# Kernel optimization log

Measured on AMD Instinct MI355X. Metric: run time of the kernel, lower is better.

## Reference

```python
import jax, jax.numpy as jnp
import numpy as np

D = 1024
H = 16
K = 32768
EPS = 1e-5


def setup_inputs() -> dict:
    key = jax.random.key(0)
    ks = jax.random.split(key, 12)
    s = 1.0 / np.sqrt(D)
    return {
        "query": jax.random.normal(ks[0], (D,), jnp.float32),
        "neighbors": jax.random.normal(ks[1], (K, D), jnp.float32),
        # nn.MultiheadAttention params
        "in_proj_w": jax.random.uniform(ks[2], (3 * D, D), jnp.float32, -s, s),
        "in_proj_b": jnp.zeros((3 * D,), jnp.float32),
        "out_proj_w": jax.random.uniform(ks[3], (D, D), jnp.float32, -s, s),
        "out_proj_b": jnp.zeros((D,), jnp.float32),
        # FFN params
        "w1": jax.random.uniform(ks[4], (4 * D, D), jnp.float32, -s, s),
        "b1": jnp.zeros((4 * D,), jnp.float32),
        "w2": jax.random.uniform(ks[5], (D, 4 * D), jnp.float32, -s, s),
        "b2": jnp.zeros((D,), jnp.float32),
        # LayerNorm params
        "g1": jnp.ones((D,), jnp.float32),
        "be1": jnp.zeros((D,), jnp.float32),
        "g2": jnp.ones((D,), jnp.float32),
        "be2": jnp.zeros((D,), jnp.float32),
    }


def _layernorm(x, g, b):
    m = jnp.mean(x, axis=-1, keepdims=True)
    v = jnp.var(x, axis=-1, keepdims=True)
    return (x - m) * jax.lax.rsqrt(v + EPS) * g + b


def reference(query, neighbors, in_proj_w, in_proj_b, out_proj_w, out_proj_b,
              w1, b1, w2, b2, g1, be1, g2, be2):
    dh = D // H
    wq, wk, wv = in_proj_w[:D], in_proj_w[D:2 * D], in_proj_w[2 * D:]
    bq, bk, bv = in_proj_b[:D], in_proj_b[D:2 * D], in_proj_b[2 * D:]

    q = (query @ wq.T + bq).reshape(H, dh)            # [H, dh]
    k = (neighbors @ wk.T + bk).reshape(K, H, dh)     # [K, H, dh]
    v = (neighbors @ wv.T + bv).reshape(K, H, dh)

    scores = jnp.einsum('hd,khd->hk', q, k) / np.sqrt(dh)  # [H, K]
    attn = jax.nn.softmax(scores, axis=-1)
    ctx = jnp.einsum('hk,khd->hd', attn, v).reshape(D)      # [D]
    attn_out = ctx @ out_proj_w.T + out_proj_b

    x = _layernorm(query + attn_out, g1, be1)
    ffn = jax.nn.gelu(x @ w1.T + b1, approximate=False) @ w2.T + b2
    return _layernorm(x + ffn, g2, be2)
```

## Files before the change

### kernel.cpp

```cpp
#include <hip/hip_runtime.h>
#include <hip/hip_bf16.h>

#define D 1024
#define H 16
#define DH 64
#define KN 32768
#define EPS 1e-5f

__device__ __forceinline__ float wave_sum(float v){
  #pragma unroll
  for (int off = 32; off; off >>= 1) v += __shfl_xor(v, off, 64);
  return v;
}

#define GLL(gp, lp) __builtin_amdgcn_global_load_lds((const __attribute__((address_space(1))) void*)(gp), (__attribute__((address_space(3))) void*)(lp), 16, 0, 0)

__global__ void g_qproj(const float* __restrict__ query, const float* __restrict__ ipw,
                        const float* __restrict__ ipb, float* __restrict__ q){
  int j = blockIdx.x, l = threadIdx.x;
  const float4* qv = (const float4*)(query + l*16);
  const float4* wv = (const float4*)(ipw + (size_t)j*D + l*16);
  float acc = 0.f;
  #pragma unroll
  for (int t = 0; t < 4; t++){
    float4 a = qv[t], b = wv[t];
    acc += a.x*b.x + a.y*b.y + a.z*b.z + a.w*b.w;
  }
  acc = wave_sum(acc);
  if (l == 0) q[j] = acc + ipb[j];
}

__global__ __launch_bounds__(256) void g_qk(const float* __restrict__ ipw, const float* __restrict__ ipb,
                                            const float* __restrict__ q, float* __restrict__ qk,
                                            float* __restrict__ sb){
  int b = blockIdx.x, t = threadIdx.x;
  int h = b >> 2, sl = b & 3;
  int jg = t >> 6, c = t & 63;
  __shared__ float qh[DH];
  __shared__ float4 red[256];
  if (t < DH) qh[t] = q[h*DH + t];
  __syncthreads();
  if (t < DH){
    float p = qh[t] * ipb[D + h*DH + t];
    p = wave_sum(p);
    if (t == 0 && sl == 0) sb[h] = p;
  }
  float4 acc = make_float4(0.f,0.f,0.f,0.f);
  for (int jj = 0; jj < 16; jj++){
    int j = jg*16 + jj;
    float4 w = *((const float4*)(ipw + (size_t)(D + h*DH + j)*D) + sl*64 + c);
    float qj = qh[j];
    acc.x += qj*w.x; acc.y += qj*w.y; acc.z += qj*w.z; acc.w += qj*w.w;
  }
  red[t] = acc;
  __syncthreads();
  if (jg == 0){
    float4 a = red[c], b1 = red[64+c], c1 = red[128+c], d1 = red[192+c];
    float4 r = make_float4(a.x+b1.x+c1.x+d1.x, a.y+b1.y+c1.y+d1.y,
                           a.z+b1.z+c1.z+d1.z, a.w+b1.w+c1.w+d1.w);
    ((float4*)(qk + h*D))[sl*64 + c] = r;
  }
}

__global__ __launch_bounds__(256, 2) void g_attn(const float* __restrict__ nbr, const float* __restrict__ qk,
                       const float* __restrict__ sb, float* __restrict__ lpart,
                       float* __restrict__ part, int rows_per_blk){
  __shared__ __align__(16) float tile[2][8*D];
  const int t = threadIdx.x;
  const int w = t >> 6, ci = t & 63;
  const int wb = t & ~63;
  const int g = (ci >> 4) & 3;
  const float sbl = sb[w*4 + g];

  float qk0[16], qk1[16], qk2[16], qk3[16];
  {
    const float4* p0 = (const float4*)(qk + (w*4+0)*D);
    const float4* p1 = (const float4*)(qk + (w*4+1)*D);
    const float4* p2 = (const float4*)(qk + (w*4+2)*D);
    const float4* p3 = (const float4*)(qk + (w*4+3)*D);
    #pragma unroll
    for (int c = 0; c < 4; c++){
      float4 f;
      f = p0[c*64 + ci]; qk0[4*c]=f.x; qk0[4*c+1]=f.y; qk0[4*c+2]=f.z; qk0[4*c+3]=f.w;
      f = p1[c*64 + ci]; qk1[4*c]=f.x; qk1[4*c+1]=f.y; qk1[4*c+2]=f.z; qk1[4*c+3]=f.w;
      f = p2[c*64 + ci]; qk2[4*c]=f.x; qk2[4*c+1]=f.y; qk2[4*c+2]=f.z; qk2[4*c+3]=f.w;
      f = p3[c*64 + ci]; qk3[4*c]=f.x; qk3[4*c+1]=f.y; qk3[4*c+2]=f.z; qk3[4*c+3]=f.w;
    }
  }
  float acc0[16], acc1[16], acc2[16], acc3[16];
  #pragma unroll
  for (int i = 0; i < 16; i++){ acc0[i]=0.f; acc1[i]=0.f; acc2[i]=0.f; acc3[i]=0.f; }
  float lsum = 0.f;

  const int k0 = blockIdx.x * rows_per_blk;
  const int ntiles = rows_per_blk >> 3;
  const uint4* gb = (const uint4*)nbr;

  {
    const uint4* gsrc = gb + (size_t)k0*256;
    #pragma unroll
    for (int i = 0; i < 8; i++) GLL(gsrc + i*256 + t, &tile[0][(i*256 + wb)*4]);
  }
  __syncthreads();

  #pragma unroll 1
  for (int tl = 0; tl < ntiles; tl++){
    int cur = tl & 1;
    if (tl + 1 < ntiles){
      const uint4* gsrc = gb + (size_t)(k0 + (tl+1)*8)*256;
      #pragma unroll
      for (int i = 0; i < 8; i++) GLL(gsrc + i*256 + t, &tile[cur^1][(i*256 + wb)*4]);
    }
    #pragma unroll 1
    for (int r = 0; r < 8; r++){
      const float4* row4 = (const float4*)(tile[cur]) + r*256;
      float xf[16];
      float s0=0.f, s1=0.f, s2=0.f, s3=0.f;
      #pragma unroll
      for (int c = 0; c < 4; c++){
        float4 a = row4[c*64 + ci];
        xf[4*c]=a.x; xf[4*c+1]=a.y; xf[4*c+2]=a.z; xf[4*c+3]=a.w;
        s0 += a.x*qk0[4*c] + a.y*qk0[4*c+1] + a.z*qk0[4*c+2] + a.w*qk0[4*c+3];
        s1 += a.x*qk1[4*c] + a.y*qk1[4*c+1] + a.z*qk1[4*c+2] + a.w*qk1[4*c+3];
        s2 += a.x*qk2[4*c] + a.y*qk2[4*c+1] + a.z*qk2[4*c+2] + a.w*qk2[4*c+3];
        s3 += a.x*qk3[4*c] + a.y*qk3[4*c+1] + a.z*qk3[4*c+2] + a.w*qk3[4*c+3];
      }
      const bool lo32 = (ci & 32) == 0;
      float za = lo32 ? s2 : s0;
      float ka = lo32 ? s0 : s2;
      float u02 = ka + __shfl_xor(za, 32, 64);
      float zb = lo32 ? s3 : s1;
      float kb = lo32 ? s1 : s3;
      float u13 = kb + __shfl_xor(zb, 32, 64);
      const bool lo16 = (ci & 16) == 0;
      float zc = lo16 ? u13 : u02;
      float kc = lo16 ? u02 : u13;
      float v = kc + __shfl_xor(zc, 16, 64);
      v += __shfl_xor(v, 8, 64);
      v += __shfl_xor(v, 4, 64);
      v += __shfl_xor(v, 2, 64);
      v += __shfl_xor(v, 1, 64);
      float pv = __expf((v + sbl)*0.125f);
      lsum += pv;
      float p0 = __shfl(pv, 0, 64);
      float p1 = __shfl(pv, 16, 64);
      float p2 = __shfl(pv, 32, 64);
      float p3 = __shfl(pv, 48, 64);
      #pragma unroll
      for (int j = 0; j < 16; j++){
        acc0[j] += p0*xf[j];
        acc1[j] += p1*xf[j];
        acc2[j] += p2*xf[j];
        acc3[j] += p3*xf[j];
      }
    }
    __syncthreads();
  }

  if ((ci & 15) == 0) lpart[blockIdx.x*H + w*4 + g] = lsum;
  float4* o = (float4*)(part + (size_t)blockIdx.x*(H*D) + (size_t)(w*4)*D);
  #pragma unroll
  for (int c = 0; c < 4; c++){
    o[0*256 + c*64 + ci] = make_float4(acc0[4*c], acc0[4*c+1], acc0[4*c+2], acc0[4*c+3]);
    o[1*256 + c*64 + ci] = make_float4(acc1[4*c], acc1[4*c+1], acc1[4*c+2], acc1[4*c+3]);
    o[2*256 + c*64 + ci] = make_float4(acc2[4*c], acc2[4*c+1], acc2[4*c+2], acc2[4*c+3]);
    o[3*256 + c*64 + ci] = make_float4(acc3[4*c], acc3[4*c+1], acc3[4*c+2], acc3[4*c+3]);
  }
}

__global__ __launch_bounds__(256) void g_red(const float* __restrict__ part, const float* __restrict__ lpart,
                                             float* __restrict__ nb, float* __restrict__ lh, int nblk){
  int b = blockIdx.x, t = threadIdx.x;
  __shared__ float red[256];
  if (b == 256){
    int h = t & 15, cs = t >> 4;
    int per = nblk >> 4;
    float s = 0.f;
    for (int k = 0; k < per; k++) s += lpart[(cs*per + k)*H + h];
    red[t] = s;
    __syncthreads();
    if (t < 16){
      float a = 0.f;
      #pragma unroll
      for (int i = 0; i < 16; i++) a += red[i*16 + t];
      lh[t] = a;
    }
    return;
  }
  int o0 = b * 64;
  int oo = t & 63, cs = t >> 6;
  int per = nblk >> 2;
  float s = 0.f;
  #pragma unroll 8
  for (int k = 0; k < per; k++) s += part[(size_t)(cs*per + k)*(H*D) + o0 + oo];
  red[t] = s;
  __syncthreads();
  if (t < 64) nb[o0 + t] = red[t] + red[64+t] + red[128+t] + red[192+t];
}

__global__ void g_ctx(const float* __restrict__ ipw, const float* __restrict__ ipb,
                      const float* __restrict__ nb, const float* __restrict__ lh,
                      float* __restrict__ ctx){
  int j = blockIdx.x, l = threadIdx.x, h = j >> 6;
  const float4* wv = (const float4*)(ipw + (size_t)(2*D + j)*D + l*16);
  const float4* nv = (const float4*)(nb + h*D + l*16);
  float acc = 0.f;
  #pragma unroll
  for (int t = 0; t < 4; t++){
    float4 b = wv[t], n = nv[t];
    acc += b.x*n.x + b.y*n.y + b.z*n.z + b.w*n.w;
  }
  acc = wave_sum(acc);
  if (l == 0) ctx[j] = acc/lh[h] + ipb[2*D + j];
}

__global__ void g_attnout(const float* __restrict__ opw, const float* __restrict__ opb,
                          const float* __restrict__ query, const float* __restrict__ ctx,
                          float* __restrict__ xb){
  int j = blockIdx.x, l = threadIdx.x;
  const float4* wv = (const float4*)(opw + (size_t)j*D + l*16);
  const float4* cv = (const float4*)(ctx + l*16);
  float acc = 0.f;
  #pragma unroll
  for (int t = 0; t < 4; t++){
    float4 b = wv[t], c = cv[t];
    acc += b.x*c.x + b.y*c.y + b.z*c.z + b.w*c.w;
  }
  acc = wave_sum(acc);
  if (l == 0) xb[j] = query[j] + acc + opb[j];
}

__global__ __launch_bounds__(256) void g_ffn1(const float* __restrict__ w1, const float* __restrict__ b1,
                                              const float* __restrict__ xb,
                                              const float* __restrict__ g1, const float* __restrict__ be1,
                                              float* __restrict__ xln, float* __restrict__ h1){
  int t = threadIdx.x, b = blockIdx.x;
  __shared__ float xs[D];
  __shared__ float red[8];
  float4 v = ((const float4*)xb)[t];
  float s = wave_sum(v.x + v.y + v.z + v.w);
  if ((t & 63) == 0) red[t >> 6] = s;
  __syncthreads();
  float m = (red[0]+red[1]+red[2]+red[3]) * (1.0f/D);
  float4 d = make_float4(v.x-m, v.y-m, v.z-m, v.w-m);
  float s2 = wave_sum(d.x*d.x + d.y*d.y + d.z*d.z + d.w*d.w);
  if ((t & 63) == 0) red[4 + (t >> 6)] = s2;
  __syncthreads();
  float var = (red[4]+red[5]+red[6]+red[7]) * (1.0f/D);
  float rs = rsqrtf(var + EPS);
  float4 gg = ((const float4*)g1)[t], bb = ((const float4*)be1)[t];
  float4 r = make_float4(d.x*rs*gg.x + bb.x, d.y*rs*gg.y + bb.y,
                         d.z*rs*gg.z + bb.z, d.w*rs*gg.w + bb.w);
  ((float4*)xs)[t] = r;
  if (b == 0) ((float4*)xln)[t] = r;
  __syncthreads();

  int w = t >> 6, l = t & 63;
  const float4* xs4 = (const float4*)xs;
  #pragma unroll 1
  for (int rr = 0; rr < 4; rr++){
    int j = b*16 + w*4 + rr;
    const float4* wr = (const float4*)(w1 + (size_t)j*D);
    float a = 0.f;
    #pragma unroll
    for (int c = 0; c < 4; c++){
      float4 ww = wr[c*64 + l], xx = xs4[c*64 + l];
      a += ww.x*xx.x + ww.y*xx.y + ww.z*xx.z + ww.w*xx.w;
    }
    a = wave_sum(a);
    if (l == 0){
      float z = a + b1[j];
      h1[j] = 0.5f*z*(1.0f + erff(z*0.70710678118654752f));
    }
  }
}

__global__ void g_ffn2(const float* __restrict__ w2, const float* __restrict__ b2v,
                       const float* __restrict__ h1, float* __restrict__ y){
  int j = blockIdx.x, l = threadIdx.x;
  const float4* wv = (const float4*)(w2 + (size_t)j*4096 + l*64);
  const float4* hv = (const float4*)(h1 + l*64);
  float acc = 0.f;
  #pragma unroll
  for (int t = 0; t < 16; t++){
    float4 b = wv[t], hh = hv[t];
    acc += b.x*hh.x + b.y*hh.y + b.z*hh.z + b.w*hh.w;
  }
  acc = wave_sum(acc);
  if (l == 0) y[j] = acc + b2v[j];
}

__global__ __launch_bounds__(1024) void g_ln2(const float* __restrict__ xln, const float* __restrict__ y,
                                              const float* __restrict__ g, const float* __restrict__ be,
                                              float* __restrict__ out){
  int t = threadIdx.x;
  __shared__ float red[16];
  __shared__ float bc;
  float v = xln[t] + y[t];
  float s = wave_sum(v);
  if ((t & 63) == 0) red[t >> 6] = s;
  __syncthreads();
  if (t == 0){ float a = 0.f; for (int i = 0; i < 16; i++) a += red[i]; bc = a*(1.0f/D); }
  __syncthreads();
  float m = bc;
  float d = v - m;
  float s2 = wave_sum(d*d);
  if ((t & 63) == 0) red[t >> 6] = s2;
  __syncthreads();
  if (t == 0){ float a = 0.f; for (int i = 0; i < 16; i++) a += red[i]; bc = a*(1.0f/D); }
  __syncthreads();
  float rs = rsqrtf(bc + EPS);
  out[t] = d*rs*g[t] + be[t];
}

extern "C" void kernel_launch(void* const* d_in, const int* in_sizes, int n_in,
                              void* d_out, int out_size, void* d_ws, size_t ws_size,
                              hipStream_t stream) {
  const float* query = (const float*)d_in[0];
  const float* nbr   = (const float*)d_in[1];
  const float* ipw   = (const float*)d_in[2];
  const float* ipb   = (const float*)d_in[3];
  const float* opw   = (const float*)d_in[4];
  const float* opb   = (const float*)d_in[5];
  const float* w1    = (const float*)d_in[6];
  const float* b1    = (const float*)d_in[7];
  const float* w2    = (const float*)d_in[8];
  const float* b2v   = (const float*)d_in[9];
  const float* g1    = (const float*)d_in[10];
  const float* be1   = (const float*)d_in[11];
  const float* g2    = (const float*)d_in[12];
  const float* be2   = (const float*)d_in[13];

  float* ws    = (float*)d_ws;
  float* q     = ws;
  float* qk    = q + D;
  float* sb    = qk + H*D;
  float* lh    = sb + 16;
  float* ctx   = lh + 16;
  float* xb    = ctx + D;
  float* xln   = xb + D;
  float* h1    = xln + D;
  float* y     = h1 + 4*D;
  float* nb    = y + D;
  float* lpart = nb + H*D;
  float* part  = lpart + 8192;

  size_t fixed_bytes = (size_t)(part - ws) * 4;
  int nblk = 512;
  while (nblk > 64 && fixed_bytes + (size_t)nblk*H*D*4 > ws_size) nblk >>= 1;
  int rows_per_blk = KN / nblk;

  g_qproj  <<<1024, 64, 0, stream>>>(query, ipw, ipb, q);
  g_qk     <<<64, 256, 0, stream>>>(ipw, ipb, q, qk, sb);
  g_attn   <<<nblk, 256, 0, stream>>>(nbr, qk, sb, lpart, part, rows_per_blk);
  g_red    <<<257, 256, 0, stream>>>(part, lpart, nb, lh, nblk);
  g_ctx    <<<1024, 64, 0, stream>>>(ipw, ipb, nb, lh, ctx);
  g_attnout<<<1024, 64, 0, stream>>>(opw, opb, query, ctx, xb);
  g_ffn1   <<<256, 256, 0, stream>>>(w1, b1, xb, g1, be1, xln, h1);
  g_ffn2   <<<1024, 64, 0, stream>>>(w2, b2v, h1, y);
  g_ln2    <<<1, 1024, 0, stream>>>(xln, y, g2, be2, (float*)d_out);
}
```

Before: 299.4 us.

## Fuse q projection into qk kernel, pair rows in attention loop, widen reduction

Merges the query projection kernel into the qk kernel, with each block recomputing its head's 64 q values, which removes one launch. The attention inner loop now handles two rows per iteration so their shuffle reductions and exps can overlap, and it raises wave priority with s_setprio around the compute. The partial-sum reduction uses 1024 threads per block instead of 256 for more parallelism over the nblk partials. The costs are redundant q computation across the 4 slice blocks of each head and higher register pressure in g_attn.

Result: slower. 306.9 us (+2.5%).

```diff
diff --git a/kernel.cpp b/kernel.cpp
--- a/kernel.cpp
+++ b/kernel.cpp
@@ -15,31 +15,41 @@
 
 #define GLL(gp, lp) __builtin_amdgcn_global_load_lds((const __attribute__((address_space(1))) void*)(gp), (__attribute__((address_space(3))) void*)(lp), 16, 0, 0)
 
-__global__ void g_qproj(const float* __restrict__ query, const float* __restrict__ ipw,
-                        const float* __restrict__ ipb, float* __restrict__ q){
-  int j = blockIdx.x, l = threadIdx.x;
-  const float4* qv = (const float4*)(query + l*16);
-  const float4* wv = (const float4*)(ipw + (size_t)j*D + l*16);
-  float acc = 0.f;
-  #pragma unroll
-  for (int t = 0; t < 4; t++){
-    float4 a = qv[t], b = wv[t];
-    acc += a.x*b.x + a.y*b.y + a.z*b.z + a.w*b.w;
-  }
-  acc = wave_sum(acc);
-  if (l == 0) q[j] = acc + ipb[j];
-}
-
-__global__ __launch_bounds__(256) void g_qk(const float* __restrict__ ipw, const float* __restrict__ ipb,
-                                            const float* __restrict__ q, float* __restrict__ qk,
-                                            float* __restrict__ sb){
+__global__ __launch_bounds__(256) void g_qk(const float* __restrict__ query,
+                                            const float* __restrict__ ipw, const float* __restrict__ ipb,
+                                            float* __restrict__ qk, float* __restrict__ sb){
   int b = blockIdx.x, t = threadIdx.x;
   int h = b >> 2, sl = b & 3;
-  int jg = t >> 6, c = t & 63;
+  int w = t >> 6, ci = t & 63;
   __shared__ float qh[DH];
   __shared__ float4 red[256];
-  if (t < DH) qh[t] = q[h*DH + t];
-  __syncthreads();
+
+  {
+    const float4* qv = (const float4*)(query + ci*16);
+    #pragma unroll 1
+    for (int jj = 0; jj < 16; jj += 2){
+      int j0 = h*DH + w*16 + jj;
+      const float4* w0 = (const float4*)(ipw + (size_t)j0*D + ci*16);
+      const float4* w1r = (const float4*)(ipw + (size_t)(j0+1)*D + ci*16);
+      float a0 = 0.f, a1 = 0.f;
+      #pragma unroll
+      for (int c = 0; c < 4; c++){
+        float4 qq = qv[c];
+        float4 x0 = w0[c];
+        float4 x1 = w1r[c];
+        a0 += x0.x*qq.x + x0.y*qq.y + x0.z*qq.z + x0.w*qq.w;
+        a1 += x1.x*qq.x + x1.y*qq.y + x1.z*qq.z + x1.w*qq.w;
+      }
+      a0 = wave_sum(a0);
+      a1 = wave_sum(a1);
+      if (ci == 0){
+        qh[w*16 + jj]     = a0 + ipb[j0];
+        qh[w*16 + jj + 1] = a1 + ipb[j0 + 1];
+      }
+    }
+  }
+  __syncthreads();
+
   if (t < DH){
     float p = qh[t] * ipb[D + h*DH + t];
     p = wave_sum(p);
@@ -47,19 +57,38 @@
   }
   float4 acc = make_float4(0.f,0.f,0.f,0.f);
   for (int jj = 0; jj < 16; jj++){
-    int j = jg*16 + jj;
-    float4 w = *((const float4*)(ipw + (size_t)(D + h*DH + j)*D) + sl*64 + c);
+    int j = w*16 + jj;
+    float4 ww = *((const float4*)(ipw + (size_t)(D + h*DH + j)*D) + sl*64 + ci);
     float qj = qh[j];
-    acc.x += qj*w.x; acc.y += qj*w.y; acc.z += qj*w.z; acc.w += qj*w.w;
+    acc.x += qj*ww.x; acc.y += qj*ww.y; acc.z += qj*ww.z; acc.w += qj*ww.w;
   }
   red[t] = acc;
   __syncthreads();
-  if (jg == 0){
-    float4 a = red[c], b1 = red[64+c], c1 = red[128+c], d1 = red[192+c];
+  if (w == 0){
+    float4 a = red[ci], b1 = red[64+ci], c1 = red[128+ci], d1 = red[192+ci];
     float4 r = make_float4(a.x+b1.x+c1.x+d1.x, a.y+b1.y+c1.y+d1.y,
                            a.z+b1.z+c1.z+d1.z, a.w+b1.w+c1.w+d1.w);
-    ((float4*)(qk + h*D))[sl*64 + c] = r;
-  }
+    ((float4*)(qk + h*D))[sl*64 + ci] = r;
+  }
+}
+
+__device__ __forceinline__ float bf4(float s0, float s1, float s2, float s3, int ci){
+  const bool lo32 = (ci & 32) == 0;
+  float za = lo32 ? s2 : s0;
+  float ka = lo32 ? s0 : s2;
+  float u02 = ka + __shfl_xor(za, 32, 64);
+  float zb = lo32 ? s3 : s1;
+  float kb = lo32 ? s1 : s3;
+  float u13 = kb + __shfl_xor(zb, 32, 64);
+  const bool lo16 = (ci & 16) == 0;
+  float zc = lo16 ? u13 : u02;
+  float kc = lo16 ? u02 : u13;
+  float v = kc + __shfl_xor(zc, 16, 64);
+  v += __shfl_xor(v, 8, 64);
+  v += __shfl_xor(v, 4, 64);
+  v += __shfl_xor(v, 2, 64);
+  v += __shfl_xor(v, 1, 64);
+  return v;
 }
 
 __global__ __launch_bounds__(256, 2) void g_attn(const float* __restrict__ nbr, const float* __restrict__ qk,
@@ -111,49 +140,49 @@
       #pragma unroll
       for (int i = 0; i < 8; i++) GLL(gsrc + i*256 + t, &tile[cur^1][(i*256 + wb)*4]);
     }
+    __builtin_amdgcn_s_setprio(1);
     #pragma unroll 1
-    for (int r = 0; r < 8; r++){
-      const float4* row4 = (const float4*)(tile[cur]) + r*256;
-      float xf[16];
-      float s0=0.f, s1=0.f, s2=0.f, s3=0.f;
+    for (int r = 0; r < 8; r += 2){
+      const float4* rowA = (const float4*)(tile[cur]) + r*256;
+      float xfA[16], xfB[16];
+      float sA0=0.f,sA1=0.f,sA2=0.f,sA3=0.f;
+      float sB0=0.f,sB1=0.f,sB2=0.f,sB3=0.f;
       #pragma unroll
       for (int c = 0; c < 4; c++){
-        float4 a = row4[c*64 + ci];
-        xf[4*c]=a.x; xf[4*c+1]=a.y; xf[4*c+2]=a.z; xf[4*c+3]=a.w;
-        s0 += a.x*qk0[4*c] + a.y*qk0[4*c+1] + a.z*qk0[4*c+2] + a.w*qk0[4*c+3];
-        s1 += a.x*qk1[4*c] + a.y*qk1[4*c+1] + a.z*qk1[4*c+2] + a.w*qk1[4*c+3];
-        s2 += a.x*qk2[4*c] + a.y*qk2[4*c+1] + a.z*qk2[4*c+2] + a.w*qk2[4*c+3];
-        s3 += a.x*qk3[4*c] + a.y*qk3[4*c+1] + a.z*qk3[4*c+2] + a.w*qk3[4*c+3];
-      }
-      const bool lo32 = (ci & 32) == 0;
-      float za = lo32 ? s2 : s0;
-      float ka = lo32 ? s0 : s2;
-      float u02 = ka + __shfl_xor(za, 32, 64);
-      float zb = lo32 ? s3 : s1;
-      float kb = lo32 ? s1 : s3;
-      float u13 = kb + __shfl_xor(zb, 32, 64);
-      const bool lo16 = (ci & 16) == 0;
-      float zc = lo16 ? u13 : u02;
-      float kc = lo16 ? u02 : u13;
-      float v = kc + __shfl_xor(zc, 16, 64);
-      v += __shfl_xor(v, 8, 64);
-      v += __shfl_xor(v, 4, 64);
-      v += __shfl_xor(v, 2, 64);
-      v += __shfl_xor(v, 1, 64);
-      float pv = __expf((v + sbl)*0.125f);
-      lsum += pv;
-      float p0 = __shfl(pv, 0, 64);
-      float p1 = __shfl(pv, 16, 64);
-      float p2 = __shfl(pv, 32, 64);
-      float p3 = __shfl(pv, 48, 64);
+        float4 a = rowA[c*64 + ci];
+        xfA[4*c]=a.x; xfA[4*c+1]=a.y; xfA[4*c+2]=a.z; xfA[4*c+3]=a.w;
+        sA0 += a.x*qk0[4*c] + a.y*qk0[4*c+1] + a.z*qk0[4*c+2] + a.w*qk0[4*c+3];
+        sA1 += a.x*qk1[4*c] + a.y*qk1[4*c+1] + a.z*qk1[4*c+2] + a.w*qk1[4*c+3];
+        sA2 += a.x*qk2[4*c] + a.y*qk2[4*c+1] + a.z*qk2[4*c+2] + a.w*qk2[4*c+3];
+        sA3 += a.x*qk3[4*c] + a.y*qk3[4*c+1] + a.z*qk3[4*c+2] + a.w*qk3[4*c+3];
+      }
+      #pragma unroll
+      for (int c = 0; c < 4; c++){
+        float4 a = rowA[256 + c*64 + ci];
+        xfB[4*c]=a.x; xfB[4*c+1]=a.y; xfB[4*c+2]=a.z; xfB[4*c+3]=a.w;
+        sB0 += a.x*qk0[4*c] + a.y*qk0[4*c+1] + a.z*qk0[4*c+2] + a.w*qk0[4*c+3];
+        sB1 += a.x*qk1[4*c] + a.y*qk1[4*c+1] + a.z*qk1[4*c+2] + a.w*qk1[4*c+3];
+        sB2 += a.x*qk2[4*c] + a.y*qk2[4*c+1] + a.z*qk2[4*c+2] + a.w*qk2[4*c+3];
+        sB3 += a.x*qk3[4*c] + a.y*qk3[4*c+1] + a.z*qk3[4*c+2] + a.w*qk3[4*c+3];
+      }
+      float vA = bf4(sA0, sA1, sA2, sA3, ci);
+      float vB = bf4(sB0, sB1, sB2, sB3, ci);
+      float pA = __expf((vA + sbl)*0.125f);
+      float pB = __expf((vB + sbl)*0.125f);
+      lsum += pA + pB;
+      float pA0 = __shfl(pA, 0, 64), pA1 = __shfl(pA, 16, 64);
+      float pA2 = __shfl(pA, 32, 64), pA3 = __shfl(pA, 48, 64);
+      float pB0 = __shfl(pB, 0, 64), pB1 = __shfl(pB, 16, 64);
+      float pB2 = __shfl(pB, 32, 64), pB3 = __shfl(pB, 48, 64);
       #pragma unroll
       for (int j = 0; j < 16; j++){
-        acc0[j] += p0*xf[j];
-        acc1[j] += p1*xf[j];
-        acc2[j] += p2*xf[j];
-        acc3[j] += p3*xf[j];
-      }
-    }
+        acc0[j] += pA0*xfA[j] + pB0*xfB[j];
+        acc1[j] += pA1*xfA[j] + pB1*xfB[j];
+        acc2[j] += pA2*xfA[j] + pB2*xfB[j];
+        acc3[j] += pA3*xfA[j] + pB3*xfB[j];
+      }
+    }
+    __builtin_amdgcn_s_setprio(0);
     __syncthreads();
   }
 
@@ -168,16 +197,17 @@
   }
 }
 
-__global__ __launch_bounds__(256) void g_red(const float* __restrict__ part, const float* __restrict__ lpart,
-                                             float* __restrict__ nb, float* __restrict__ lh, int nblk){
+__global__ __launch_bounds__(1024) void g_red(const float* __restrict__ part, const float* __restrict__ lpart,
+                                              float* __restrict__ nb, float* __restrict__ lh, int nblk){
   int b = blockIdx.x, t = threadIdx.x;
-  __shared__ float red[256];
+  __shared__ float red[1024];
   if (b == 256){
-    int h = t & 15, cs = t >> 4;
-    int per = nblk >> 4;
-    float s = 0.f;
-    for (int k = 0; k < per; k++) s += lpart[(cs*per + k)*H + h];
-    red[t] = s;
+    if (t < 256){
+      int hh = t & 15, cs = t >> 4, per = nblk >> 4;
+      float s = 0.f;
+      for (int k = 0; k < per; k++) s += lpart[(cs*per + k)*H + hh];
+      red[t] = s;
+    }
     __syncthreads();
     if (t < 16){
       float a = 0.f;
@@ -189,13 +219,18 @@
   }
   int o0 = b * 64;
   int oo = t & 63, cs = t >> 6;
-  int per = nblk >> 2;
+  int per = nblk >> 4;
   float s = 0.f;
   #pragma unroll 8
   for (int k = 0; k < per; k++) s += part[(size_t)(cs*per + k)*(H*D) + o0 + oo];
   red[t] = s;
   __syncthreads();
-  if (t < 64) nb[o0 + t] = red[t] + red[64+t] + red[128+t] + red[192+t];
+  if (t < 64){
+    float a = 0.f;
+    #pragma unroll
+    for (int i = 0; i < 16; i++) a += red[i*64 + t];
+    nb[o0 + t] = a;
+  }
 }
 
 __global__ void g_ctx(const float* __restrict__ ipw, const float* __restrict__ ipb,
@@ -332,8 +367,7 @@
   const float* be2   = (const float*)d_in[13];
 
   float* ws    = (float*)d_ws;
-  float* q     = ws;
-  float* qk    = q + D;
+  float* qk    = ws;
   float* sb    = qk + H*D;
   float* lh    = sb + 16;
   float* ctx   = lh + 16;
@@ -350,10 +384,9 @@
   while (nblk > 64 && fixed_bytes + (size_t)nblk*H*D*4 > ws_size) nblk >>= 1;
   int rows_per_blk = KN / nblk;
 
-  g_qproj  <<<1024, 64, 0, stream>>>(query, ipw, ipb, q);
-  g_qk     <<<64, 256, 0, stream>>>(ipw, ipb, q, qk, sb);
+  g_qk     <<<64, 256, 0, stream>>>(query, ipw, ipb, qk, sb);
   g_attn   <<<nblk, 256, 0, stream>>>(nbr, qk, sb, lpart, part, rows_per_blk);
-  g_red    <<<257, 256, 0, stream>>>(part, lpart, nb, lh, nblk);
+  g_red    <<<257, 1024, 0, stream>>>(part, lpart, nb, lh, nblk);
   g_ctx    <<<1024, 64, 0, stream>>>(ipw, ipb, nb, lh, ctx);
   g_attnout<<<1024, 64, 0, stream>>>(opw, opb, query, ctx, xb);
   g_ffn1   <<<256, 256, 0, stream>>>(w1, b1, xb, g1, be1, xln, h1);
```
